# Kernel optimization log

Measured on AMD Instinct MI355X. Metric: run time of the kernel, lower is better.

## Reference

```python
import jax, jax.numpy as jnp
import numpy as np

B, N, F_IN, H, L, C = 64, 512, 21, 64, 3, 9
NEG_INF = -jnp.inf


def setup_inputs() -> dict:
    key = jax.random.key(0)
    ks = jax.random.split(key, 24)
    s = lambda shape, k, scale=0.05: jax.random.normal(ks[k], shape, dtype=jnp.float32) * scale
    return {
        "node_features": jax.random.normal(ks[0], (B, N, F_IN), dtype=jnp.float32),
        "adjacency": jax.random.bernoulli(ks[1], 0.05, (B, N, N)).astype(jnp.float32),
        "node_mask": jnp.ones((B, N), dtype=bool),
        "We": s((F_IN, H), 2), "be": jnp.zeros((H,), jnp.float32),
        "Wl": s((L, H, H), 3), "a_src": s((L, H), 4), "a_dst": s((L, H), 5),
        "gamma": jnp.ones((L, H), jnp.float32), "beta": jnp.zeros((L, H), jnp.float32),
        "P1": s((H, H), 6), "pb1": jnp.zeros((H,), jnp.float32),
        "P2": s((H,), 7), "pb2": jnp.zeros((), jnp.float32),
        "C1": s((H, H), 8), "cb1": jnp.zeros((H,), jnp.float32),
        "C2": s((H, C), 9), "cb2": jnp.zeros((C,), jnp.float32),
    }


def _layernorm(x, g, b, eps=1e-5):
    mu = x.mean(-1, keepdims=True)
    var = ((x - mu) ** 2).mean(-1, keepdims=True)
    return (x - mu) * jax.lax.rsqrt(var + eps) * g + b


def reference(node_features, adjacency, node_mask, We, be, Wl, a_src, a_dst,
              gamma, beta, P1, pb1, P2, pb2, C1, cb1, C2, cb2):
    # node embedding (dropout = identity in eval)
    h = jax.nn.relu(node_features @ We + be)  # [B,N,H]
    adj_zero = adjacency == 0
    for l in range(L):
        hW = h @ Wl[l]                                  # [B,N,H]
        attn = hW @ a_src[l]                            # [B,N] src scores
        attn = attn[:, :, None] + (hW @ a_dst[l])[:, None, :]  # [B,N,N]
        attn = jax.nn.leaky_relu(attn, 0.2)
        attn = jnp.where(adj_zero, NEG_INF, attn)
        attn = jnp.nan_to_num(jax.nn.softmax(attn, axis=-1), nan=0.0)
        h = _layernorm(h + attn @ hW, gamma[l], beta[l])
    # attention pooling
    pa = jnp.tanh(h @ P1 + pb1) @ P2 + pb2              # [B,N]
    pa = jnp.where(node_mask, pa, NEG_INF)
    pa = jnp.nan_to_num(jax.nn.softmax(pa, axis=-1), nan=0.0)
    g = jnp.einsum('bn,bnh->bh', pa, h)                 # [B,H]
    return jax.nn.relu(g @ C1 + cb1) @ C2 + cb2         # [B,C]
```

## Files before the change

### kernel.cpp

```cpp
#include <hip/hip_runtime.h>


#define WS_H     0
#define WS_HWA   2097152
#define WS_HWB   4194304
#define WS_SA    6291456
#define WS_TA    6324224
#define WS_SB    6356992
#define WS_TB    6389760
#define WS_PA    6422528
#define WS_DEG   6455296
#define WS_LIST_BYTES 25952256

typedef const __attribute__((address_space(1))) unsigned int gu32;
typedef __attribute__((address_space(3))) unsigned int lu32;

__device__ __forceinline__ void gl_lds16(const float* g, float* l) {
  __builtin_amdgcn_global_load_lds((gu32*)g, (lu32*)l, 16, 0, 0);
}

template <int CTRL>
__device__ __forceinline__ float dpp_add(float v) {
  int x = __builtin_amdgcn_update_dpp(0, __float_as_int(v), CTRL, 0xf, 0xf, true);
  return v + __int_as_float(x);
}
__device__ __forceinline__ float wtot(float v) {
  v = dpp_add<0x111>(v);
  v = dpp_add<0x112>(v);
  v = dpp_add<0x114>(v);
  v = dpp_add<0x118>(v);
  v = dpp_add<0x142>(v);
  v = dpp_add<0x143>(v);
  return __int_as_float(__builtin_amdgcn_readlane(__float_as_int(v), 63));
}
__device__ __forceinline__ float rsum16d(float v) {
  v = dpp_add<0x111>(v);
  v = dpp_add<0x112>(v);
  v = dpp_add<0x114>(v);
  v = dpp_add<0x118>(v);
  return v;
}
__device__ __forceinline__ float bcastf(float v, int l) {
  return __int_as_float(__builtin_amdgcn_readlane(__float_as_int(v), l));
}

__device__ __forceinline__ float wsum(float v) {
#pragma unroll
  for (int o = 32; o; o >>= 1) v += __shfl_xor(v, o, 64);
  return v;
}
__device__ __forceinline__ float wmax(float v) {
#pragma unroll
  for (int o = 32; o; o >>= 1) v = fmaxf(v, __shfl_xor(v, o, 64));
  return v;
}

__global__ __launch_bounds__(512, 4) void k_embed_hw(
    const float* __restrict__ x, const float* __restrict__ We,
    const float* __restrict__ be, const float* __restrict__ adj,
    const float* __restrict__ W0, const float* __restrict__ asrc,
    const float* __restrict__ adst,
    float* __restrict__ h, int* __restrict__ deg,
    unsigned short* __restrict__ nlist,
    float* __restrict__ hW, float* __restrict__ s, float* __restrict__ t) {
  __shared__ float lw[64 * 64];
  __shared__ unsigned short lidx[8][4][64];
  int tid = threadIdx.x, lane = tid & 63, wv = tid >> 6;
  int blk = blockIdx.x;
  int xcd = blk & 7, i = blk >> 3;
  int b = xcd * 8 + (i & 7), sub = i >> 3;
  int rb = b * 512 + sub * 32 + wv * 4;
#pragma unroll
  for (int k = 0; k < 2; ++k)
    *(float4*)&lw[k * 2048 + tid * 4] = *(const float4*)&W0[k * 2048 + tid * 4];
  float wreg[21];
#pragma unroll
  for (int f = 0; f < 21; ++f) wreg[f] = We[f * 64 + lane];
  float bev = be[lane];
  unsigned long long lmask = (1ull << lane) - 1ull;
  float4 a0[4], a1[4];
#pragma unroll
  for (int r = 0; r < 4; ++r) {
    const float4* ar = (const float4*)(adj + (size_t)(rb + r) * 512);
    a0[r] = ar[lane];
    a1[r] = ar[64 + lane];
  }
  float hst[4];
#pragma unroll
  for (int r = 0; r < 4; ++r) {
    int row = rb + r;
    const float* xr = x + (size_t)row * 21;
    float acc = bev;
#pragma unroll
    for (int f = 0; f < 21; ++f) acc = fmaf(xr[f], wreg[f], acc);
    acc = fmaxf(acc, 0.0f);
    h[(size_t)row * 64 + lane] = acc;
    hst[r] = acc;
    float comp[8] = {a0[r].x, a0[r].y, a0[r].z, a0[r].w,
                     a1[r].x, a1[r].y, a1[r].z, a1[r].w};
    int cnt = 0;
#pragma unroll
    for (int c = 0; c < 8; ++c) {
      bool on = comp[c] != 0.0f;
      unsigned long long m = __ballot(on);
      if (on) {
        int pos = cnt + __popcll(m & lmask);
        int col = (c < 4) ? (lane * 4 + c) : (256 + lane * 4 + (c - 4));
        if (pos < 64) lidx[wv][r][pos] = (unsigned short)col;
      }
      cnt += __popcll(m);
    }
    if (lane == 0) deg[row] = cnt < 64 ? cnt : 64;
  }
  {
    ushort4 v = *(ushort4*)&lidx[wv][0][lane * 4];
    *(ushort4*)(nlist + (size_t)rb * 64 + lane * 4) = v;
  }
  __syncthreads();
  float av = asrc[lane], dv = adst[lane];
  float acc[4] = {};
#pragma unroll 8
  for (int c = 0; c < 64; ++c) {
    float wrow = lw[c * 64 + lane];
#pragma unroll
    for (int r = 0; r < 4; ++r)
      acc[r] = fmaf(bcastf(hst[r], c), wrow, acc[r]);
  }
#pragma unroll
  for (int r = 0; r < 4; ++r) {
    int row = rb + r;
    hW[(size_t)row * 64 + lane] = acc[r];
    float ps = wtot(acc[r] * av);
    float pt = wtot(acc[r] * dv);
    if (lane == 0) { s[row] = ps; t[row] = pt; }
  }
}

template <int MODE>
__global__ __launch_bounds__(1024) void k_layer(
    float* __restrict__ h, const float* __restrict__ hWin,
    const float* __restrict__ sIn, const float* __restrict__ tIn,
    const int* __restrict__ deg, const unsigned short* __restrict__ nlist,
    const float* __restrict__ gamma, const float* __restrict__ beta,
    const float* __restrict__ Wn, const float* __restrict__ v1,
    const float* __restrict__ v2,
    float* __restrict__ hWout, float* __restrict__ sOut,
    float* __restrict__ tOut) {
  __shared__ float hlds[512 * 64];
  __shared__ float lw[64 * 68];
  __shared__ float tlds[512];
  int tid = threadIdx.x, lane = tid & 63, wv = tid >> 6;
  int blk = blockIdx.x;
  int b = (blk & 7) * 8 + ((blk >> 3) & 7);
  int sub = blk >> 6;
  int base = b * 512 + sub * 128;
  int rb = base + wv * 8;

  unsigned short jr[8]; float sir[8], hrr[8]; int dgr[8];
#pragma unroll
  for (int r = 0; r < 8; ++r) {
    int row = rb + r;
    jr[r] = nlist[(size_t)row * 64 + lane];
    sir[r] = sIn[row];
    hrr[r] = h[(size_t)row * 64 + lane];
    dgr[r] = deg[row];
  }
  {
    int rr = tid >> 4, q = tid & 15;
    *(float4*)&lw[rr * 68 + q * 4] = *(const float4*)&Wn[rr * 64 + q * 4];
  }
  const float* tb = tIn + ((size_t)b << 9);
  if (tid < 128) *(float4*)&tlds[tid * 4] = *(const float4*)&tb[tid * 4];
  {
    const char* src = (const char*)(hWin + ((size_t)b << 9) * 64);
    char* dst = (char*)hlds;
#pragma unroll
    for (int c = 0; c < 8; ++c) {
      int off = wv * 8192 + c * 1024;
      gl_lds16((const float*)(src + off + lane * 16), (float*)(dst + off));
    }
  }
  __syncthreads();

  float gm = gamma[lane], bt = beta[lane];
  float hst[8];
#pragma unroll
  for (int r = 0; r < 8; ++r) {
    int dgs = __builtin_amdgcn_readfirstlane(dgr[r]);
    bool act = lane < dgs;
    int jm = act ? (int)jr[r] : 0;
    float tv = act ? tlds[jm] : 0.0f;
    float e = sir[r] + tv;
    e = e > 0.0f ? e : 0.2f * e;
    float wj = act ? __expf(e) : 0.0f;
    int bits = __float_as_int(wj) & ~511;
    int packed = bits | jm;
    float wq = __int_as_float(bits);
    float acc0 = 0.0f, acc1 = 0.0f;
    int dg8 = (dgs + 7) & ~7;
    for (int n = 0; n < dg8; n += 8) {
#pragma unroll
      for (int k = 0; k < 8; k += 2) {
        int u0 = __builtin_amdgcn_readlane(packed, n + k);
        int u1 = __builtin_amdgcn_readlane(packed, n + k + 1);
        acc0 = fmaf(__int_as_float(u0 & ~511),
                    hlds[(u0 & 511) * 64 + lane], acc0);
        acc1 = fmaf(__int_as_float(u1 & ~511),
                    hlds[(u1 & 511) * 64 + lane], acc1);
      }
    }
    float dsum = wtot(wq);
    float a = dgs > 0 ? (acc0 + acc1) * (1.0f / dsum) : 0.0f;
    float xv = hrr[r] + a;
    float s1 = wtot(xv), s2 = wtot(xv * xv);
    float mu = s1 * 0.015625f;
    float var = fmaf(-mu, mu, s2 * 0.015625f);
    float hn = fmaf((xv - mu) * rsqrtf(var + 1e-5f), gm, bt);
    h[(size_t)(rb + r) * 64 + lane] = hn;
    hst[r] = hn;
  }
  __syncthreads();
  float* lhT = hlds;
#pragma unroll
  for (int r = 0; r < 8; ++r) lhT[lane * 132 + (wv * 8 + r)] = hst[r];
  __syncthreads();
  int tc = tid & 15, tr = tid >> 4;
  float acc[2][4] = {};
#pragma unroll 4
  for (int c = 0; c < 64; ++c) {
    float2 aa = *(const float2*)&lhT[c * 132 + tr * 2];
    float4 bb = *(const float4*)&lw[c * 68 + tc * 4];
    float av2[2] = {aa.x, aa.y};
    float bv[4] = {bb.x, bb.y, bb.z, bb.w};
#pragma unroll
    for (int ii = 0; ii < 2; ++ii)
#pragma unroll
      for (int j = 0; j < 4; ++j)
        acc[ii][j] = fmaf(av2[ii], bv[j], acc[ii][j]);
  }
  float p1[4], p2[4];
#pragma unroll
  for (int j = 0; j < 4; ++j) { p1[j] = v1[tc * 4 + j]; p2[j] = v2[tc * 4 + j]; }
#pragma unroll
  for (int ii = 0; ii < 2; ++ii) {
    int row = base + tr * 2 + ii;
    if (MODE == 0) {
      *(float4*)&hWout[(size_t)row * 64 + tc * 4] =
          make_float4(acc[ii][0], acc[ii][1], acc[ii][2], acc[ii][3]);
      float ps = acc[ii][0] * p1[0] + acc[ii][1] * p1[1] +
                 acc[ii][2] * p1[2] + acc[ii][3] * p1[3];
      float pt = acc[ii][0] * p2[0] + acc[ii][1] * p2[1] +
                 acc[ii][2] * p2[2] + acc[ii][3] * p2[3];
      ps = rsum16d(ps);
      pt = rsum16d(pt);
      if (tc == 15) { sOut[row] = ps; tOut[row] = pt; }
    } else {
      float p = 0.0f;
#pragma unroll
      for (int j = 0; j < 4; ++j) p += tanhf(acc[ii][j] + p1[j]) * p2[j];
      p = rsum16d(p);
      if (tc == 15) sOut[row] = p;
    }
  }
}

__global__ __launch_bounds__(512) void k_pool(const float* __restrict__ h,
    const float* __restrict__ pa, const float* __restrict__ C1,
    const float* __restrict__ cb1, const float* __restrict__ C2,
    const float* __restrict__ cb2, float* __restrict__ out) {
  __shared__ float red[8];
  __shared__ float gpart[8][64];
  __shared__ float gl[64], rl[64];
  int b = ((blockIdx.x & 7) << 3) | (blockIdx.x >> 3);
  int tid = threadIdx.x, lane = tid & 63, wv = tid >> 6;
  float v = pa[b * 512 + tid];
  float m = wmax(v);
  if (lane == 0) red[wv] = m;
  __syncthreads();
  float bm = red[0];
#pragma unroll
  for (int w = 1; w < 8; ++w) bm = fmaxf(bm, red[w]);
  float e = __expf(v - bm);
  float sm = wsum(e);
  __syncthreads();
  if (lane == 0) red[wv] = sm;
  __syncthreads();
  float bs = 0.0f;
#pragma unroll
  for (int w = 0; w < 8; ++w) bs += red[w];
  float p = e / bs;
  const float* hb = h + ((size_t)b * 512) * 64;
  float g = 0.0f;
#pragma unroll
  for (int l = 0; l < 64; ++l) {
    float pj = __shfl(p, l, 64);
    g = fmaf(pj, hb[(size_t)(wv * 64 + l) * 64 + lane], g);
  }
  gpart[wv][lane] = g;
  __syncthreads();
  if (wv == 0) {
    float gg = 0.0f;
#pragma unroll
    for (int w = 0; w < 8; ++w) gg += gpart[w][lane];
    gl[lane] = gg;
    float rr = cb1[lane];
#pragma unroll
    for (int j = 0; j < 64; ++j) rr = fmaf(gl[j], C1[j * 64 + lane], rr);
    rr = fmaxf(rr, 0.0f);
    rl[lane] = rr;
    if (lane < 9) {
      float o = cb2[lane];
#pragma unroll
      for (int k = 0; k < 64; ++k) o = fmaf(rl[k], C2[k * 9 + lane], o);
      out[b * 9 + lane] = o;
    }
  }
}

extern "C" void kernel_launch(void* const* d_in, const int* in_sizes, int n_in,
                              void* d_out, int out_size, void* d_ws, size_t ws_size,
                              hipStream_t stream) {
  const float* x    = (const float*)d_in[0];
  const float* adj  = (const float*)d_in[1];
  const float* We   = (const float*)d_in[3];
  const float* be   = (const float*)d_in[4];
  const float* Wl   = (const float*)d_in[5];
  const float* asrc = (const float*)d_in[6];
  const float* adst = (const float*)d_in[7];
  const float* gamma= (const float*)d_in[8];
  const float* beta = (const float*)d_in[9];
  const float* P1   = (const float*)d_in[10];
  const float* pb1  = (const float*)d_in[11];
  const float* P2   = (const float*)d_in[12];
  const float* C1   = (const float*)d_in[14];
  const float* cb1  = (const float*)d_in[15];
  const float* C2   = (const float*)d_in[16];
  const float* cb2  = (const float*)d_in[17];
  float* out = (float*)d_out;

  float* ws  = (float*)d_ws;
  float* h   = ws + WS_H;
  float* hwA = ws + WS_HWA;
  float* hwB = ws + WS_HWB;
  float* sA  = ws + WS_SA;
  float* tA  = ws + WS_TA;
  float* sB  = ws + WS_SB;
  float* tB  = ws + WS_TB;
  float* pa  = ws + WS_PA;
  int*   deg = (int*)(ws + WS_DEG);
  unsigned short* nlist = (unsigned short*)((char*)d_ws + WS_LIST_BYTES);

  k_embed_hw<<<1024, 512, 0, stream>>>(x, We, be, adj, Wl, asrc, adst,
                                       h, deg, nlist, hwA, sA, tA);
  k_layer<0><<<256, 1024, 0, stream>>>(h, hwA, sA, tA, deg, nlist,
                                       gamma, beta, Wl + 4096,
                                       asrc + 64, adst + 64, hwB, sB, tB);
  k_layer<0><<<256, 1024, 0, stream>>>(h, hwB, sB, tB, deg, nlist,
                                       gamma + 64, beta + 64, Wl + 8192,
                                       asrc + 128, adst + 128, hwA, sA, tA);
  k_layer<1><<<256, 1024, 0, stream>>>(h, hwA, sA, tA, deg, nlist,
                                       gamma + 128, beta + 128, P1, pb1, P2,
                                       nullptr, pa, nullptr);
  k_pool<<<64, 512, 0, stream>>>(h, pa, C1, cb1, C2, cb2, out);
}
```

Measured before the change: 225.6 us.

## Tile embed projection via LDS transpose and interleave two rows in layer gather

The embedding kernel now writes h transposed into shared memory and computes hW with a 2D thread tiling (16 column groups of 4 outputs), in place of per-lane readlane broadcasts. The attention logits are reduced with a 16-lane DPP sum, and the launch-bounds occupancy hint is dropped. In the layer kernel, two rows are processed together so their neighbor-gather loops interleave, exposing more independent LDS loads and FMAs. The cost is extra LDS traffic and register pressure, plus some divergence-free but uneven work when the two rows have different degrees.

```diff
diff --git a/kernel.cpp b/kernel.cpp
--- a/kernel.cpp
+++ b/kernel.cpp
@@ -40,9 +40,6 @@
   v = dpp_add<0x118>(v);
   return v;
 }
-__device__ __forceinline__ float bcastf(float v, int l) {
-  return __int_as_float(__builtin_amdgcn_readlane(__float_as_int(v), l));
-}
 
 __device__ __forceinline__ float wsum(float v) {
 #pragma unroll
@@ -55,7 +52,7 @@
   return v;
 }
 
-__global__ __launch_bounds__(512, 4) void k_embed_hw(
+__global__ __launch_bounds__(512) void k_embed_hw(
     const float* __restrict__ x, const float* __restrict__ We,
     const float* __restrict__ be, const float* __restrict__ adj,
     const float* __restrict__ W0, const float* __restrict__ asrc,
@@ -63,16 +60,21 @@
     float* __restrict__ h, int* __restrict__ deg,
     unsigned short* __restrict__ nlist,
     float* __restrict__ hW, float* __restrict__ s, float* __restrict__ t) {
-  __shared__ float lw[64 * 64];
+  __shared__ float lw[64 * 68];
+  __shared__ float lhT[64 * 33];
   __shared__ unsigned short lidx[8][4][64];
   int tid = threadIdx.x, lane = tid & 63, wv = tid >> 6;
   int blk = blockIdx.x;
   int xcd = blk & 7, i = blk >> 3;
   int b = xcd * 8 + (i & 7), sub = i >> 3;
-  int rb = b * 512 + sub * 32 + wv * 4;
-#pragma unroll
-  for (int k = 0; k < 2; ++k)
-    *(float4*)&lw[k * 2048 + tid * 4] = *(const float4*)&W0[k * 2048 + tid * 4];
+  int base = b * 512 + sub * 32;
+  int rb = base + wv * 4;
+#pragma unroll
+  for (int k = 0; k < 2; ++k) {
+    int idx = tid + 512 * k;
+    int rr = idx >> 4, q = idx & 15;
+    *(float4*)&lw[rr * 68 + q * 4] = *(const float4*)&W0[rr * 64 + q * 4];
+  }
   float wreg[21];
 #pragma unroll
   for (int f = 0; f < 21; ++f) wreg[f] = We[f * 64 + lane];
@@ -85,7 +87,6 @@
     a0[r] = ar[lane];
     a1[r] = ar[64 + lane];
   }
-  float hst[4];
 #pragma unroll
   for (int r = 0; r < 4; ++r) {
     int row = rb + r;
@@ -95,7 +96,7 @@
     for (int f = 0; f < 21; ++f) acc = fmaf(xr[f], wreg[f], acc);
     acc = fmaxf(acc, 0.0f);
     h[(size_t)row * 64 + lane] = acc;
-    hst[r] = acc;
+    lhT[lane * 33 + (wv * 4 + r)] = acc;
     float comp[8] = {a0[r].x, a0[r].y, a0[r].z, a0[r].w,
                      a1[r].x, a1[r].y, a1[r].z, a1[r].w};
     int cnt = 0;
@@ -117,23 +118,28 @@
     *(ushort4*)(nlist + (size_t)rb * 64 + lane * 4) = v;
   }
   __syncthreads();
-  float av = asrc[lane], dv = adst[lane];
+  int tc = tid & 15, tr = tid >> 4;
   float acc[4] = {};
 #pragma unroll 8
   for (int c = 0; c < 64; ++c) {
-    float wrow = lw[c * 64 + lane];
-#pragma unroll
-    for (int r = 0; r < 4; ++r)
-      acc[r] = fmaf(bcastf(hst[r], c), wrow, acc[r]);
-  }
-#pragma unroll
-  for (int r = 0; r < 4; ++r) {
-    int row = rb + r;
-    hW[(size_t)row * 64 + lane] = acc[r];
-    float ps = wtot(acc[r] * av);
-    float pt = wtot(acc[r] * dv);
-    if (lane == 0) { s[row] = ps; t[row] = pt; }
-  }
+    float a = lhT[c * 33 + tr];
+    float4 bb = *(const float4*)&lw[c * 68 + tc * 4];
+    acc[0] = fmaf(a, bb.x, acc[0]);
+    acc[1] = fmaf(a, bb.y, acc[1]);
+    acc[2] = fmaf(a, bb.z, acc[2]);
+    acc[3] = fmaf(a, bb.w, acc[3]);
+  }
+  float p1[4], p2[4];
+#pragma unroll
+  for (int j = 0; j < 4; ++j) { p1[j] = asrc[tc * 4 + j]; p2[j] = adst[tc * 4 + j]; }
+  int row = base + tr;
+  *(float4*)&hW[(size_t)row * 64 + tc * 4] =
+      make_float4(acc[0], acc[1], acc[2], acc[3]);
+  float ps = acc[0] * p1[0] + acc[1] * p1[1] + acc[2] * p1[2] + acc[3] * p1[3];
+  float pt = acc[0] * p2[0] + acc[1] * p2[1] + acc[2] * p2[2] + acc[3] * p2[3];
+  ps = rsum16d(ps);
+  pt = rsum16d(pt);
+  if (tc == 15) { s[row] = ps; t[row] = pt; }
 }
 
 template <int MODE>
@@ -185,39 +191,64 @@
   float gm = gamma[lane], bt = beta[lane];
   float hst[8];
 #pragma unroll
-  for (int r = 0; r < 8; ++r) {
-    int dgs = __builtin_amdgcn_readfirstlane(dgr[r]);
-    bool act = lane < dgs;
-    int jm = act ? (int)jr[r] : 0;
-    float tv = act ? tlds[jm] : 0.0f;
-    float e = sir[r] + tv;
-    e = e > 0.0f ? e : 0.2f * e;
-    float wj = act ? __expf(e) : 0.0f;
-    int bits = __float_as_int(wj) & ~511;
-    int packed = bits | jm;
-    float wq = __int_as_float(bits);
-    float acc0 = 0.0f, acc1 = 0.0f;
-    int dg8 = (dgs + 7) & ~7;
-    for (int n = 0; n < dg8; n += 8) {
-#pragma unroll
-      for (int k = 0; k < 8; k += 2) {
-        int u0 = __builtin_amdgcn_readlane(packed, n + k);
-        int u1 = __builtin_amdgcn_readlane(packed, n + k + 1);
-        acc0 = fmaf(__int_as_float(u0 & ~511),
-                    hlds[(u0 & 511) * 64 + lane], acc0);
-        acc1 = fmaf(__int_as_float(u1 & ~511),
-                    hlds[(u1 & 511) * 64 + lane], acc1);
+  for (int rp = 0; rp < 8; rp += 2) {
+    int dgA = __builtin_amdgcn_readfirstlane(dgr[rp]);
+    int dgB = __builtin_amdgcn_readfirstlane(dgr[rp + 1]);
+    bool actA = lane < dgA, actB = lane < dgB;
+    int jmA = actA ? (int)jr[rp] : 0;
+    int jmB = actB ? (int)jr[rp + 1] : 0;
+    float eA = sir[rp] + (actA ? tlds[jmA] : 0.0f);
+    float eB = sir[rp + 1] + (actB ? tlds[jmB] : 0.0f);
+    eA = eA > 0.0f ? eA : 0.2f * eA;
+    eB = eB > 0.0f ? eB : 0.2f * eB;
+    float wjA = actA ? __expf(eA) : 0.0f;
+    float wjB = actB ? __expf(eB) : 0.0f;
+    int bitsA = __float_as_int(wjA) & ~511;
+    int bitsB = __float_as_int(wjB) & ~511;
+    int pkA = bitsA | jmA, pkB = bitsB | jmB;
+    float a0A = 0.0f, a1A = 0.0f, a0B = 0.0f, a1B = 0.0f;
+    int mA = (dgA + 7) & ~7, mB = (dgB + 7) & ~7;
+    int mx = mA > mB ? mA : mB;
+    for (int n = 0; n < mx; n += 8) {
+      if (n < mA) {
+#pragma unroll
+        for (int k = 0; k < 8; k += 2) {
+          int u0 = __builtin_amdgcn_readlane(pkA, n + k);
+          int u1 = __builtin_amdgcn_readlane(pkA, n + k + 1);
+          a0A = fmaf(__int_as_float(u0 & ~511),
+                     hlds[(u0 & 511) * 64 + lane], a0A);
+          a1A = fmaf(__int_as_float(u1 & ~511),
+                     hlds[(u1 & 511) * 64 + lane], a1A);
+        }
       }
-    }
-    float dsum = wtot(wq);
-    float a = dgs > 0 ? (acc0 + acc1) * (1.0f / dsum) : 0.0f;
-    float xv = hrr[r] + a;
-    float s1 = wtot(xv), s2 = wtot(xv * xv);
-    float mu = s1 * 0.015625f;
-    float var = fmaf(-mu, mu, s2 * 0.015625f);
-    float hn = fmaf((xv - mu) * rsqrtf(var + 1e-5f), gm, bt);
-    h[(size_t)(rb + r) * 64 + lane] = hn;
-    hst[r] = hn;
+      if (n < mB) {
+#pragma unroll
+        for (int k = 0; k < 8; k += 2) {
+          int u0 = __builtin_amdgcn_readlane(pkB, n + k);
+          int u1 = __builtin_amdgcn_readlane(pkB, n + k + 1);
+          a0B = fmaf(__int_as_float(u0 & ~511),
+                     hlds[(u0 & 511) * 64 + lane], a0B);
+          a1B = fmaf(__int_as_float(u1 & ~511),
+                     hlds[(u1 & 511) * 64 + lane], a1B);
+        }
+      }
+    }
+    float dsumA = wtot(__int_as_float(bitsA));
+    float dsumB = wtot(__int_as_float(bitsB));
+    float aA = dgA > 0 ? (a0A + a1A) * (1.0f / dsumA) : 0.0f;
+    float aB = dgB > 0 ? (a0B + a1B) * (1.0f / dsumB) : 0.0f;
+    float xvA = hrr[rp] + aA, xvB = hrr[rp + 1] + aB;
+    float s1A = wtot(xvA), s2A = wtot(xvA * xvA);
+    float s1B = wtot(xvB), s2B = wtot(xvB * xvB);
+    float muA = s1A * 0.015625f, muB = s1B * 0.015625f;
+    float varA = fmaf(-muA, muA, s2A * 0.015625f);
+    float varB = fmaf(-muB, muB, s2B * 0.015625f);
+    float hnA = fmaf((xvA - muA) * rsqrtf(varA + 1e-5f), gm, bt);
+    float hnB = fmaf((xvB - muB) * rsqrtf(varB + 1e-5f), gm, bt);
+    h[(size_t)(rb + rp) * 64 + lane] = hnA;
+    h[(size_t)(rb + rp + 1) * 64 + lane] = hnB;
+    hst[rp] = hnA;
+    hst[rp + 1] = hnB;
   }
   __syncthreads();
   float* lhT = hlds;
```

Measured after the change: 220.6 us. 2.2% less time.
